# Optimization experiments

Hardware: AMD Instinct MI355X
Metric: run time of the kernel (lower is better)

Reference implementation:

```python
import jax, jax.numpy as jnp
import numpy as np

N = 1048576
D = 128
C = 1000
MOMENTUM = 0.95


def setup_inputs() -> dict:
    key = jax.random.key(0)
    k1, k2, k3, k4 = jax.random.split(key, 4)
    feats = jax.random.normal(k1, (N, D), dtype=jnp.float32)
    labels = jax.random.randint(k2, (N,), 0, C, dtype=jnp.int64)
    weights = jax.random.uniform(k3, (N,), dtype=jnp.float32)
    proto = jax.random.normal(k4, (C, D), dtype=jnp.float32)  # buffer [C, d]
    return {"feats": feats, "labels": labels, "weights": weights, "proto": proto}


def reference(feats, labels, weights, proto):
    # Per-class weighted mean via a single segment reduction (replaces the
    # per-class masked loop in the torch module), then fused EMA update.
    labels = labels.astype(jnp.int32)
    # [C, d] sum of w_i * f_i per class
    wsum_feats = jax.ops.segment_sum(weights[:, None] * feats, labels, num_segments=C)
    # [C] sum of weights per class
    wsum = jax.ops.segment_sum(weights, labels, num_segments=C)
    vec = wsum_feats / jnp.maximum(wsum, 1e-8)[:, None]  # [C, d]
    present = (wsum > 0.0)[:, None]  # classes seen in this batch
    new_proto = jnp.where(present, MOMENTUM * proto + (1.0 - MOMENTUM) * vec, proto)
    return new_proto
```

## Files before the change

kernel.cpp:

```cpp
#include <hip/hip_runtime.h>

#define NROWS 1048576
#define DIM   128
#define NCLS  1000
#define NBLK  256
#define RPB   4096
#define RPT   16
#define MOM   0.95f


__global__ __launch_bounds__(256) void k_hist(const int* __restrict__ labels,
                                              unsigned* __restrict__ total,
                                              unsigned* __restrict__ blockCnt)
{
    __shared__ unsigned h[NCLS];
    const int tid = threadIdx.x;
    const int b   = blockIdx.x;
    for (int c = tid; c < NCLS; c += 256) h[c] = 0u;
    __syncthreads();
    const int base = b * RPB;
#pragma unroll
    for (int k = 0; k < RPT; ++k)
        atomicAdd(&h[labels[base + k * 256 + tid]], 1u);
    __syncthreads();
    for (int c = tid; c < NCLS; c += 256) {
        const unsigned cnt = h[c];
        blockCnt[b * 1024 + c] = cnt;
        if (cnt) atomicAdd(&total[c], cnt);
    }
}

__global__ __launch_bounds__(1024) void k_scan(const unsigned* __restrict__ total,
                                               unsigned* __restrict__ classBase)
{
    __shared__ unsigned s[1024];
    const int tid = threadIdx.x;
    unsigned v = (tid < NCLS) ? total[tid] : 0u;
    s[tid] = v;
    __syncthreads();
    for (int off = 1; off < 1024; off <<= 1) {
        unsigned u = (tid >= off) ? s[tid - off] : 0u;
        __syncthreads();
        s[tid] += u;
        __syncthreads();
    }
    if (tid < NCLS) classBase[tid] = s[tid] - v;
}

__global__ __launch_bounds__(256) void k_scanB(const unsigned* __restrict__ blockCnt,
                                               const unsigned* __restrict__ classBase,
                                               unsigned* __restrict__ blockBase)
{
    __shared__ unsigned s[256];
    const int c = blockIdx.x;
    const int t = threadIdx.x;
    unsigned v = blockCnt[t * 1024 + c];
    s[t] = v;
    __syncthreads();
    for (int off = 1; off < 256; off <<= 1) {
        unsigned u = (t >= off) ? s[t - off] : 0u;
        __syncthreads();
        s[t] += u;
        __syncthreads();
    }
    blockBase[t * 1024 + c] = classBase[c] + (s[t] - v);
}

__global__ __launch_bounds__(256) void k_scatter(const int* __restrict__ labels,
                                                 const unsigned* __restrict__ blockBase,
                                                 unsigned* __restrict__ perm)
{
    __shared__ unsigned off_lds[NCLS];
    __shared__ unsigned basec[NCLS];
    const int tid = threadIdx.x;
    const int b   = blockIdx.x;
    for (int c = tid; c < NCLS; c += 256) {
        basec[c]   = blockBase[b * 1024 + c];
        off_lds[c] = 0u;
    }
    __syncthreads();
    const int base = b * RPB;
#pragma unroll
    for (int k = 0; k < RPT; ++k) {
        const int r = base + k * 256 + tid;
        const int c = labels[r];
        unsigned o = atomicAdd(&off_lds[c], 1u);
        perm[basec[c] + o] = (unsigned)r;
    }
}

__global__ __launch_bounds__(512) void k_reduce(
        const float*    __restrict__ feats,
        const float*    __restrict__ weights,
        const float*    __restrict__ proto,
        const unsigned* __restrict__ perm,
        const unsigned* __restrict__ total,
        const unsigned* __restrict__ classBase,
        float* __restrict__ out)
{
    const int c      = blockIdx.x;
    const int tid    = threadIdx.x;
    const int lane32 = tid & 31;
    const int grp    = tid >> 5;
    const int n      = (int)total[c];
    const unsigned base = classBase[c];
    const float4* __restrict__ f4 = (const float4*)feats;

    float4 acc = make_float4(0.f, 0.f, 0.f, 0.f);
    float  wacc = 0.f;

    int i = grp;
    for (; i + 112 < n; i += 128) {
        unsigned r[8]; float w[8]; float4 f[8];
#pragma unroll
        for (int u = 0; u < 8; ++u) r[u] = perm[base + i + u * 16];
#pragma unroll
        for (int u = 0; u < 8; ++u) w[u] = weights[r[u]];
#pragma unroll
        for (int u = 0; u < 8; ++u) f[u] = f4[(long)r[u] * 32 + lane32];
#pragma unroll
        for (int u = 0; u < 8; ++u) {
            acc.x += w[u] * f[u].x; acc.y += w[u] * f[u].y;
            acc.z += w[u] * f[u].z; acc.w += w[u] * f[u].w;
            wacc  += w[u];
        }
    }
    for (; i < n; i += 16) {
        unsigned r = perm[base + i];
        float w = weights[r];
        float4 f = f4[(long)r * 32 + lane32];
        acc.x += w * f.x; acc.y += w * f.y; acc.z += w * f.z; acc.w += w * f.w;
        wacc += w;
    }

    __shared__ float4 sAcc[16][32];
    __shared__ float  sW[16];
    sAcc[grp][lane32] = acc;
    if (lane32 == 0) sW[grp] = wacc;
    __syncthreads();

    if (grp == 0) {
        float4 t = sAcc[0][lane32];
#pragma unroll
        for (int g = 1; g < 16; ++g) {
            float4 a = sAcc[g][lane32];
            t.x += a.x; t.y += a.y; t.z += a.z; t.w += a.w;
        }
        float ws = 0.f;
#pragma unroll
        for (int g = 0; g < 16; ++g) ws += sW[g];

        const float4 p = ((const float4*)proto)[c * 32 + lane32];
        float4 o;
        if (ws > 0.f) {
            const float den = fmaxf(ws, 1e-8f);
            o.x = MOM * p.x + 0.05f * (t.x / den);
            o.y = MOM * p.y + 0.05f * (t.y / den);
            o.z = MOM * p.z + 0.05f * (t.z / den);
            o.w = MOM * p.w + 0.05f * (t.w / den);
        } else {
            o = p;
        }
        ((float4*)out)[c * 32 + lane32] = o;
    }
}

extern "C" void kernel_launch(void* const* d_in, const int* in_sizes, int n_in,
                              void* d_out, int out_size, void* d_ws, size_t ws_size,
                              hipStream_t stream)
{
    const float* feats   = (const float*)d_in[0];
    const int*   labels  = (const int*)  d_in[1];
    const float* weights = (const float*)d_in[2];
    const float* proto   = (const float*)d_in[3];
    float* out = (float*)d_out;

    unsigned* total     = (unsigned*)d_ws;
    unsigned* classBase = total + 1024;
    unsigned* blockCnt  = classBase + 1024;
    unsigned* blockBase = blockCnt + NBLK * 1024;
    unsigned* perm      = blockBase + NBLK * 1024;

    hipMemsetAsync(total, 0, 1024 * sizeof(unsigned), stream);
    k_hist   <<<NBLK, 256, 0, stream>>>(labels, total, blockCnt);
    k_scan   <<<1, 1024, 0, stream>>>(total, classBase);
    k_scanB  <<<NCLS, 256, 0, stream>>>(blockCnt, classBase, blockBase);
    k_scatter<<<NBLK, 256, 0, stream>>>(labels, blockBase, perm);
    k_reduce <<<NCLS, 512, 0, stream>>>(feats, weights, proto, perm,
                                        total, classBase, out);
}
```

Measured before the change: 729.4 us.

## Stage scatter through LDS for class-sorted writes; shrink reduce blocks to 256 threads

The scatter kernel now builds a local counting sort in shared memory. It computes per-block class offsets with a scan, places indices into an LDS buffer, and then writes perm in class-contiguous order, so global writes are coalesced instead of random. The reduce kernel drops from 512 to 256 threads with a 4-way unroll instead of 8-way, which changes occupancy and the memory-level parallelism available for the gather. The histogram arrays are padded to 1024 entries. The cost is more LDS per scatter block, about 30KB, plus extra syncs.

```diff
diff --git a/kernel.cpp b/kernel.cpp
--- a/kernel.cpp
+++ b/kernel.cpp
@@ -13,17 +13,17 @@
                                               unsigned* __restrict__ total,
                                               unsigned* __restrict__ blockCnt)
 {
-    __shared__ unsigned h[NCLS];
+    __shared__ unsigned h[1024];
     const int tid = threadIdx.x;
     const int b   = blockIdx.x;
-    for (int c = tid; c < NCLS; c += 256) h[c] = 0u;
+    for (int c = tid; c < 1024; c += 256) h[c] = 0u;
     __syncthreads();
     const int base = b * RPB;
 #pragma unroll
     for (int k = 0; k < RPT; ++k)
         atomicAdd(&h[labels[base + k * 256 + tid]], 1u);
     __syncthreads();
-    for (int c = tid; c < NCLS; c += 256) {
+    for (int c = tid; c < 1024; c += 256) {
         const unsigned cnt = h[c];
         blockCnt[b * 1024 + c] = cnt;
         if (cnt) atomicAdd(&total[c], cnt);
@@ -70,26 +70,65 @@
                                                  const unsigned* __restrict__ blockBase,
                                                  unsigned* __restrict__ perm)
 {
-    __shared__ unsigned off_lds[NCLS];
-    __shared__ unsigned basec[NCLS];
+    __shared__ unsigned h[1024];
+    __shared__ unsigned localBase[1024];
+    __shared__ unsigned basec[1024];
+    __shared__ unsigned tsum[256];
+    __shared__ unsigned s_perm[RPB];
+    __shared__ unsigned short s_cls[RPB];
+
     const int tid = threadIdx.x;
     const int b   = blockIdx.x;
-    for (int c = tid; c < NCLS; c += 256) {
-        basec[c]   = blockBase[b * 1024 + c];
-        off_lds[c] = 0u;
-    }
-    __syncthreads();
+
+    for (int c = tid; c < 1024; c += 256) {
+        h[c]     = 0u;
+        basec[c] = blockBase[b * 1024 + c];
+    }
+    __syncthreads();
+
     const int base = b * RPB;
+    int lab[RPT];
 #pragma unroll
     for (int k = 0; k < RPT; ++k) {
-        const int r = base + k * 256 + tid;
-        const int c = labels[r];
-        unsigned o = atomicAdd(&off_lds[c], 1u);
-        perm[basec[c] + o] = (unsigned)r;
-    }
-}
-
-__global__ __launch_bounds__(512) void k_reduce(
+        lab[k] = labels[base + k * 256 + tid];
+        atomicAdd(&h[lab[k]], 1u);
+    }
+    __syncthreads();
+
+    const unsigned a0 = h[4*tid], a1 = h[4*tid+1], a2 = h[4*tid+2], a3 = h[4*tid+3];
+    const unsigned ts = a0 + a1 + a2 + a3;
+    tsum[tid] = ts;
+    __syncthreads();
+    for (int off = 1; off < 256; off <<= 1) {
+        unsigned u = (tid >= off) ? tsum[tid - off] : 0u;
+        __syncthreads();
+        tsum[tid] += u;
+        __syncthreads();
+    }
+    const unsigned eb = tsum[tid] - ts;
+    localBase[4*tid]   = eb;
+    localBase[4*tid+1] = eb + a0;
+    localBase[4*tid+2] = eb + a0 + a1;
+    localBase[4*tid+3] = eb + a0 + a1 + a2;
+    h[4*tid] = 0u; h[4*tid+1] = 0u; h[4*tid+2] = 0u; h[4*tid+3] = 0u;
+    __syncthreads();
+
+#pragma unroll
+    for (int k = 0; k < RPT; ++k) {
+        const int c = lab[k];
+        const unsigned pos = localBase[c] + atomicAdd(&h[c], 1u);
+        s_perm[pos] = (unsigned)(base + k * 256 + tid);
+        s_cls[pos]  = (unsigned short)c;
+    }
+    __syncthreads();
+
+    for (int pos = tid; pos < RPB; pos += 256) {
+        const int c = s_cls[pos];
+        perm[basec[c] + (pos - localBase[c])] = s_perm[pos];
+    }
+}
+
+__global__ __launch_bounds__(256) void k_reduce(
         const float*    __restrict__ feats,
         const float*    __restrict__ weights,
         const float*    __restrict__ proto,
@@ -110,22 +149,24 @@
     float  wacc = 0.f;
 
     int i = grp;
-    for (; i + 112 < n; i += 128) {
-        unsigned r[8]; float w[8]; float4 f[8];
-#pragma unroll
-        for (int u = 0; u < 8; ++u) r[u] = perm[base + i + u * 16];
-#pragma unroll
-        for (int u = 0; u < 8; ++u) w[u] = weights[r[u]];
-#pragma unroll
-        for (int u = 0; u < 8; ++u) f[u] = f4[(long)r[u] * 32 + lane32];
-#pragma unroll
-        for (int u = 0; u < 8; ++u) {
-            acc.x += w[u] * f[u].x; acc.y += w[u] * f[u].y;
-            acc.z += w[u] * f[u].z; acc.w += w[u] * f[u].w;
-            wacc  += w[u];
-        }
-    }
-    for (; i < n; i += 16) {
+    for (; i + 24 < n; i += 32) {
+        unsigned r0 = perm[base + i];
+        unsigned r1 = perm[base + i + 8];
+        unsigned r2 = perm[base + i + 16];
+        unsigned r3 = perm[base + i + 24];
+        float w0 = weights[r0], w1 = weights[r1];
+        float w2 = weights[r2], w3 = weights[r3];
+        float4 f0 = f4[(long)r0 * 32 + lane32];
+        float4 f1 = f4[(long)r1 * 32 + lane32];
+        float4 f2 = f4[(long)r2 * 32 + lane32];
+        float4 f3 = f4[(long)r3 * 32 + lane32];
+        acc.x += w0 * f0.x; acc.y += w0 * f0.y; acc.z += w0 * f0.z; acc.w += w0 * f0.w;
+        acc.x += w1 * f1.x; acc.y += w1 * f1.y; acc.z += w1 * f1.z; acc.w += w1 * f1.w;
+        acc.x += w2 * f2.x; acc.y += w2 * f2.y; acc.z += w2 * f2.z; acc.w += w2 * f2.w;
+        acc.x += w3 * f3.x; acc.y += w3 * f3.y; acc.z += w3 * f3.z; acc.w += w3 * f3.w;
+        wacc += w0 + w1 + w2 + w3;
+    }
+    for (; i < n; i += 8) {
         unsigned r = perm[base + i];
         float w = weights[r];
         float4 f = f4[(long)r * 32 + lane32];
@@ -133,8 +174,8 @@
         wacc += w;
     }
 
-    __shared__ float4 sAcc[16][32];
-    __shared__ float  sW[16];
+    __shared__ float4 sAcc[8][32];
+    __shared__ float  sW[8];
     sAcc[grp][lane32] = acc;
     if (lane32 == 0) sW[grp] = wacc;
     __syncthreads();
@@ -142,13 +183,13 @@
     if (grp == 0) {
         float4 t = sAcc[0][lane32];
 #pragma unroll
-        for (int g = 1; g < 16; ++g) {
+        for (int g = 1; g < 8; ++g) {
             float4 a = sAcc[g][lane32];
             t.x += a.x; t.y += a.y; t.z += a.z; t.w += a.w;
         }
         float ws = 0.f;
 #pragma unroll
-        for (int g = 0; g < 16; ++g) ws += sW[g];
+        for (int g = 0; g < 8; ++g) ws += sW[g];
 
         const float4 p = ((const float4*)proto)[c * 32 + lane32];
         float4 o;
@@ -186,6 +227,6 @@
     k_scan   <<<1, 1024, 0, stream>>>(total, classBase);
     k_scanB  <<<NCLS, 256, 0, stream>>>(blockCnt, classBase, blockBase);
     k_scatter<<<NBLK, 256, 0, stream>>>(labels, blockBase, perm);
-    k_reduce <<<NCLS, 512, 0, stream>>>(feats, weights, proto, perm,
+    k_reduce <<<NCLS, 256, 0, stream>>>(feats, weights, proto, perm,
                                         total, classBase, out);
 }
```

After: 717.6 us. Within noise of the previous version (-1.6%).
